# Performance work log

Hardware: AMD Instinct MI355X
Metric: run time of the kernel (lower is better)

Reference implementation:

```python
import jax, jax.numpy as jnp
import numpy as np

N = 10000
E = 160000
D_IN = 128
H = 1024
NUM_GRAPHS = 8
EPS = 1e-5


def setup_inputs() -> dict:
    key = jax.random.key(0)
    ks = jax.random.split(key, 24)
    x = jax.random.normal(ks[0], (N, D_IN), dtype=jnp.float32)
    edge_index = jax.random.randint(ks[1], (2, E), 0, N, dtype=jnp.int32)
    batch = jnp.sort(jax.random.randint(ks[2], (N,), 0, NUM_GRAPHS, dtype=jnp.int32))
    s = 0.02
    W1 = jax.random.normal(ks[3], (D_IN, H), dtype=jnp.float32) * s
    b1 = jnp.zeros((H,), jnp.float32)
    Wh = jax.random.normal(ks[4], (3, H, H), dtype=jnp.float32) * s
    bh = jnp.zeros((3, H), jnp.float32)
    ln_g = jnp.ones((4, H), jnp.float32)
    ln_b = jnp.zeros((4, H), jnp.float32)
    vW = jax.random.normal(ks[5], (6, H, H), dtype=jnp.float32) * s
    vb = jnp.zeros((6, H), jnp.float32)
    vWo = jax.random.normal(ks[6], (H, 1), dtype=jnp.float32) * s
    vbo = jnp.zeros((1,), jnp.float32)
    return {"x": x, "edge_index": edge_index, "batch": batch,
            "W1": W1, "b1": b1, "Wh": Wh, "bh": bh,
            "ln_g": ln_g, "ln_b": ln_b, "vW": vW, "vb": vb,
            "vWo": vWo, "vbo": vbo}


def _layer_norm(x, g, b):
    m = jnp.mean(x, axis=-1, keepdims=True)
    v = jnp.mean(jnp.square(x - m), axis=-1, keepdims=True)
    return (x - m) * jax.lax.rsqrt(v + EPS) * g + b


def reference(x, edge_index, batch, W1, b1, Wh, bh, ln_g, ln_b, vW, vb, vWo, vbo):
    # GCNConv: add self loops, symmetric normalization, x @ W, scatter-add at dst, + bias
    loops = jnp.arange(N, dtype=edge_index.dtype)
    src = jnp.concatenate([edge_index[0], loops])
    dst = jnp.concatenate([edge_index[1], loops])
    deg = jax.ops.segment_sum(jnp.ones_like(dst, dtype=x.dtype), dst, num_segments=N)
    dinv = jax.lax.rsqrt(jnp.maximum(deg, 1.0))
    norm = (dinv[src] * dinv[dst])[:, None]  # [E+N, 1]

    def gcn(h, W, b):
        h = h @ W                              # [N, H]
        msg = h[src] * norm                    # gather + scale [E+N, H]
        return jax.ops.segment_sum(msg, dst, num_segments=N) + b

    x1 = gcn(x, W1, b1)
    h = jax.nn.relu(_layer_norm(x1, ln_g[0], ln_b[0]))
    x2 = gcn(h, Wh[0], bh[0])
    h = jax.nn.relu(_layer_norm(x2 + x1, ln_g[1], ln_b[1]))
    x3 = gcn(h, Wh[1], bh[1])
    h = jax.nn.relu(_layer_norm(x3 + x1, ln_g[2], ln_b[2]))
    x4 = gcn(h, Wh[2], bh[2])
    node_embeddings = jax.nn.relu(_layer_norm(x4 + h, ln_g[3], ln_b[3]))

    # global mean pool per graph
    counts = jax.ops.segment_sum(jnp.ones((N,), x.dtype), batch, num_segments=NUM_GRAPHS)
    sums = jax.ops.segment_sum(node_embeddings, batch, num_segments=NUM_GRAPHS)
    graph_embedding = sums / jnp.maximum(counts, 1.0)[:, None]

    v = graph_embedding
    for i in range(6):
        v = jax.nn.relu(v @ vW[i] + vb[i])
    state_value = (v @ vWo + vbo).squeeze(-1)
    return node_embeddings, graph_embedding, state_value
```

## Files before the change

### kernel.cpp

```cpp
#include <hip/hip_runtime.h>
#include <stdint.h>

#define N_NODES 10000
#define E_EDGES 160000
#define DIN 128
#define H 1024
#define NUM_GRAPHS 8
#define LN_EPS 1e-5f

typedef unsigned short u16;
typedef __attribute__((ext_vector_type(8))) short short8;
typedef __attribute__((ext_vector_type(8))) unsigned short ushort8v;
typedef __attribute__((ext_vector_type(4))) float f32x4;

__device__ __forceinline__ float bf2f(u16 v) { return __uint_as_float(((unsigned)v) << 16); }
__device__ __forceinline__ u16 f2bf(float f) {
    unsigned u = __float_as_uint(f);
    u += 0x7fffu + ((u >> 16) & 1u);
    return (u16)(u >> 16);
}

__global__ void k_init(int* cnt, int* goff, float* __restrict__ gsum,
                       float* __restrict__ vbuf, const float* __restrict__ vb,
                       float* __restrict__ sbufs) {
    int i = blockIdx.x * 256 + threadIdx.x;
    if (i < N_NODES) cnt[i] = 0;
    if (i <= NUM_GRAPHS) goff[i] = 0;
    if (i < NUM_GRAPHS * H) gsum[i] = 0.f;
    if (i < 6 * H) {
        int il = i >> 10, j = i & (H - 1);
        float b = vb[il * H + j];
        float* base = vbuf + (size_t)(il + 1) * NUM_GRAPHS * H;
#pragma unroll
        for (int g = 0; g < NUM_GRAPHS; g++) base[g * H + j] = b;
    }
    for (int j = i; j < 3 * N_NODES * 2; j += 40 * 256) sbufs[j] = 0.f;
}

__global__ void k_setup(const int* __restrict__ dst, int* __restrict__ cnt,
                        const int* __restrict__ batch, int* __restrict__ goff,
                        const float* __restrict__ x, u16* __restrict__ xb) {
    int i = blockIdx.x * 256 + threadIdx.x;
    if (i < E_EDGES) atomicAdd(&cnt[dst[i]], 1);
    if (i < N_NODES) {
        int b0 = batch[i];
        int b1 = (i + 1 < N_NODES) ? batch[i + 1] : NUM_GRAPHS;
        for (int g = b0 + 1; g <= b1; g++) goff[g] = i + 1;
    }
    if (i < N_NODES * DIN) xb[i] = f2bf(x[i]);
}

__global__ __launch_bounds__(1024) void k_scan(const int* __restrict__ cnt, int* __restrict__ offs,
                                               int* __restrict__ cursor, float* __restrict__ dinv) {
    __shared__ int wsum[16];
    __shared__ int carry_s;
    int tid = threadIdx.x;
    int lane = tid & 63, wv = tid >> 6;
    if (tid == 0) carry_s = 0;
    __syncthreads();
    for (int base = 0; base < N_NODES; base += 1024) {
        int i = base + tid;
        int v = (i < N_NODES) ? cnt[i] : 0;
        int x = v;
#pragma unroll
        for (int off = 1; off < 64; off <<= 1) {
            int t = __shfl_up(x, off);
            if (lane >= off) x += t;
        }
        if (lane == 63) wsum[wv] = x;
        __syncthreads();
        int carry = carry_s;
        if (wv == 0) {
            int ws = (lane < 16) ? wsum[lane] : 0;
#pragma unroll
            for (int off = 1; off < 16; off <<= 1) {
                int t = __shfl_up(ws, off);
                if (lane >= off) ws += t;
            }
            if (lane < 16) wsum[lane] = ws;
        }
        __syncthreads();
        int wbase = (wv > 0) ? wsum[wv - 1] : 0;
        int incl = wbase + x;
        int excl = incl - v;
        if (i < N_NODES) {
            offs[i] = carry + excl;
            cursor[i] = carry + excl;
            dinv[i] = rsqrtf((float)(v + 1));
        }
        if (tid == 1023) carry_s = carry + incl;
        __syncthreads();
    }
    if (tid == 0) offs[N_NODES] = carry_s;
}

__global__ void k_fill(const int* __restrict__ src, const int* __restrict__ dst,
                       int* __restrict__ cursor, int* __restrict__ csr_src) {
    int e = blockIdx.x * 256 + threadIdx.x;
    if (e < E_EDGES) {
        int d = dst[e];
        int slot = atomicAdd(&cursor[d], 1);
        csr_src[slot] = src[e];
    }
}

__global__ void k_wprep(const float* __restrict__ W1, const float* __restrict__ Wh,
                        u16* __restrict__ Wt1, u16* __restrict__ Wt3) {
    __shared__ float tile[32][33];
    int z = blockIdx.z;
    const float* src;
    u16* dst;
    int R;
    if (z == 0) {
        if (blockIdx.y * 32 >= DIN) return;
        src = W1; dst = Wt1; R = DIN;
    } else {
        src = Wh + (size_t)(z - 1) * H * H;
        dst = Wt3 + (size_t)(z - 1) * H * H;
        R = H;
    }
    const int C = H;
    int tx = threadIdx.x, ty = threadIdx.y;
    int x = blockIdx.x * 32 + tx;
#pragma unroll
    for (int i = 0; i < 32; i += 8) {
        int y = blockIdx.y * 32 + ty + i;
        tile[ty + i][tx] = (y < R && x < C) ? src[(size_t)y * C + x] : 0.f;
    }
    __syncthreads();
    int xo = blockIdx.y * 32 + tx;
#pragma unroll
    for (int i = 0; i < 32; i += 8) {
        int yo = blockIdx.x * 32 + ty + i;
        if (yo < C && xo < R) dst[(size_t)yo * R + xo] = f2bf(tile[tx][ty + i]);
    }
}

__global__ __launch_bounds__(64) void k_agg_x(const u16* __restrict__ xb, const float* __restrict__ dinv,
                                              const int* __restrict__ offs, const int* __restrict__ csr_src,
                                              u16* __restrict__ xa) {
    __shared__ float s_dv[64];
    __shared__ int s_id[64];
    int d = blockIdx.x;
    int tid = threadIdx.x;
    int c = tid * 2;
    float dd = dinv[d];
    float a0, a1;
    {
        unsigned v = *(const unsigned*)(xb + (size_t)d * DIN + c);
        a0 = dd * bf2f((u16)(v & 0xffffu));
        a1 = dd * bf2f((u16)(v >> 16));
    }
    int beg = offs[d], end = offs[d + 1];
    for (int chunk = beg; chunk < end; chunk += 64) {
        int nthis = end - chunk;
        if (nthis > 64) nthis = 64;
        int np = (nthis + 7) & ~7;
        __syncthreads();
        if (tid < nthis) {
            int s = csr_src[chunk + tid];
            s_id[tid] = s;
            s_dv[tid] = dinv[s];
        } else if (tid < np) {
            s_id[tid] = d;
            s_dv[tid] = 0.f;
        }
        __syncthreads();
        for (int i = 0; i < np; i += 8) {
            unsigned v[8];
            float e[8];
#pragma unroll
            for (int u = 0; u < 8; u++) {
                int s = s_id[i + u];
                e[u] = s_dv[i + u];
                v[u] = *(const unsigned*)(xb + (size_t)s * DIN + c);
            }
#pragma unroll
            for (int u = 0; u < 8; u++) {
                a0 += e[u] * bf2f((u16)(v[u] & 0xffffu));
                a1 += e[u] * bf2f((u16)(v[u] >> 16));
            }
        }
    }
    a0 *= dd;
    a1 *= dd;
    unsigned o = ((unsigned)f2bf(a1) << 16) | (unsigned)f2bf(a0);
    *(unsigned*)(xa + (size_t)d * DIN + c) = o;
}

__global__ __launch_bounds__(128) void k_ln1(const u16* __restrict__ t, const float* __restrict__ bias,
                                             const float* __restrict__ gamma, const float* __restrict__ beta,
                                             u16* __restrict__ out_bf, u16* __restrict__ out_pre) {
    __shared__ float red1[2], red2[2];
    int d = blockIdx.x;
    int tid = threadIdx.x;
    int c = tid * 8;
    float x[8];
    {
        ushort8v v = *(const ushort8v*)(t + (size_t)d * H + c);
#pragma unroll
        for (int i = 0; i < 8; i++) x[i] = bf2f(v[i]) + bias[c + i];
    }
    {
        ushort8v p;
#pragma unroll
        for (int i = 0; i < 8; i++) p[i] = f2bf(x[i]);
        *(ushort8v*)(out_pre + (size_t)d * H + c) = p;
    }
    float s1 = 0.f, s2 = 0.f;
#pragma unroll
    for (int i = 0; i < 8; i++) { s1 += x[i]; s2 += x[i] * x[i]; }
#pragma unroll
    for (int off = 32; off > 0; off >>= 1) {
        s1 += __shfl_down(s1, off);
        s2 += __shfl_down(s2, off);
    }
    int lane = tid & 63, wv = tid >> 6;
    if (lane == 0) { red1[wv] = s1; red2[wv] = s2; }
    __syncthreads();
    float sum = red1[0] + red1[1];
    float ssq = red2[0] + red2[1];
    float mean = sum * (1.f / H);
    float var = fmaxf(ssq * (1.f / H) - mean * mean, 0.f);
    float inv = rsqrtf(var + LN_EPS);
    ushort8v o;
#pragma unroll
    for (int i = 0; i < 8; i++)
        o[i] = f2bf(fmaxf((x[i] - mean) * inv * gamma[c + i] + beta[c + i], 0.f));
    *(ushort8v*)(out_bf + (size_t)d * H + c) = o;
}

__global__ __launch_bounds__(256) void k_agg_col(const u16* __restrict__ t, const u16* __restrict__ resid,
                                                 const float* __restrict__ bias, const float* __restrict__ dinv,
                                                 const int* __restrict__ offs, const int* __restrict__ csr_src,
                                                 u16* __restrict__ abuf, float* __restrict__ sbuf) {
    int chunk = blockIdx.x & 7;
    int grp = threadIdx.x >> 4;
    int ln = threadIdx.x & 15;
    int d = (blockIdx.x >> 3) * 16 + grp;
    int col = chunk * 128 + ln * 8;
    const u16* tc = t + col;
    float dd = dinv[d];
    float a[8];
    {
        ushort8v v = *(const ushort8v*)(tc + (size_t)d * H);
#pragma unroll
        for (int i = 0; i < 8; i++) a[i] = dd * bf2f(v[i]);
    }
    int e = offs[d], end = offs[d + 1];
    for (; e + 8 <= end; e += 8) {
        int s[8];
        float w[8];
        ushort8v vv[8];
#pragma unroll
        for (int u = 0; u < 8; u++) s[u] = csr_src[e + u];
#pragma unroll
        for (int u = 0; u < 8; u++) {
            w[u] = dinv[s[u]];
            vv[u] = *(const ushort8v*)(tc + (size_t)s[u] * H);
        }
#pragma unroll
        for (int u = 0; u < 8; u++)
#pragma unroll
            for (int j = 0; j < 8; j++) a[j] += w[u] * bf2f(vv[u][j]);
    }
    for (; e + 2 <= end; e += 2) {
        int s0 = csr_src[e], s1 = csr_src[e + 1];
        float w0 = dinv[s0], w1 = dinv[s1];
        ushort8v v0 = *(const ushort8v*)(tc + (size_t)s0 * H);
        ushort8v v1 = *(const ushort8v*)(tc + (size_t)s1 * H);
#pragma unroll
        for (int j = 0; j < 8; j++) a[j] += w0 * bf2f(v0[j]) + w1 * bf2f(v1[j]);
    }
    if (e < end) {
        int s0 = csr_src[e];
        float w0 = dinv[s0];
        ushort8v v0 = *(const ushort8v*)(tc + (size_t)s0 * H);
#pragma unroll
        for (int j = 0; j < 8; j++) a[j] += w0 * bf2f(v0[j]);
    }
    float x[8];
    {
        ushort8v r = *(const ushort8v*)(resid + (size_t)d * H + col);
#pragma unroll
        for (int i = 0; i < 8; i++) x[i] = dd * a[i] + bias[col + i] + bf2f(r[i]);
    }
    ushort8v o;
#pragma unroll
    for (int i = 0; i < 8; i++) o[i] = f2bf(x[i]);
    *(ushort8v*)(abuf + (size_t)d * H + col) = o;
    float s1 = 0.f, s2 = 0.f;
#pragma unroll
    for (int i = 0; i < 8; i++) { s1 += x[i]; s2 += x[i] * x[i]; }
#pragma unroll
    for (int off = 1; off < 16; off <<= 1) {
        s1 += __shfl_xor(s1, off);
        s2 += __shfl_xor(s2, off);
    }
    if (ln == 0) {
        atomicAdd(&sbuf[d * 2], s1);
        atomicAdd(&sbuf[d * 2 + 1], s2);
    }
}

template <int MODE>
__global__ __launch_bounds__(256) void k_ln_apply(const u16* __restrict__ abuf, const float* __restrict__ sbuf,
                                                  const float* __restrict__ gamma, const float* __restrict__ beta,
                                                  u16* __restrict__ out_bf, float* __restrict__ out_f32) {
    int chunk = blockIdx.x & 7;
    int grp = threadIdx.x >> 4;
    int ln = threadIdx.x & 15;
    int d = (blockIdx.x >> 3) * 16 + grp;
    int col = chunk * 128 + ln * 8;
    float mean = sbuf[d * 2] * (1.f / H);
    float var = fmaxf(sbuf[d * 2 + 1] * (1.f / H) - mean * mean, 0.f);
    float inv = rsqrtf(var + LN_EPS);
    ushort8v v = *(const ushort8v*)(abuf + (size_t)d * H + col);
    float y[8];
#pragma unroll
    for (int i = 0; i < 8; i++)
        y[i] = fmaxf((bf2f(v[i]) - mean) * inv * gamma[col + i] + beta[col + i], 0.f);
    if (MODE == 2) {
        float4 o0 = {y[0], y[1], y[2], y[3]};
        float4 o1 = {y[4], y[5], y[6], y[7]};
        *(float4*)(out_f32 + (size_t)d * H + col) = o0;
        *(float4*)(out_f32 + (size_t)d * H + col + 4) = o1;
    } else {
        ushort8v o;
#pragma unroll
        for (int i = 0; i < 8; i++) o[i] = f2bf(y[i]);
        *(ushort8v*)(out_bf + (size_t)d * H + col) = o;
    }
}

typedef __attribute__((address_space(1))) const unsigned int gas_u32;
typedef __attribute__((address_space(3))) unsigned int las_u32;
__device__ __forceinline__ void gld_lds16(const void* g, void* l) {
    __builtin_amdgcn_global_load_lds((gas_u32*)g, (las_u32*)l, 16, 0, 0);
}

__global__ __launch_bounds__(256) void k_gemm(const u16* __restrict__ A, const u16* __restrict__ B,
                                              u16* __restrict__ C, int M, int Nn, int K) {
    __shared__ __align__(16) u16 sA[2][128 * 32];
    __shared__ __align__(16) u16 sB[2][128 * 32];
    int mtiles = (M + 127) >> 7;
    int L = blockIdx.x;
    int cls = L & 7;
    int s = L >> 3;
    int nt = s & 7;
    int mt = (s >> 3) * 8 + cls;
    if (mt >= mtiles) return;
    int m0 = mt << 7;
    int n0 = nt << 7;

    int tid = threadIdx.x;
    int lane = tid & 63;
    int w = tid >> 6;
    int wm = w >> 1, wn = w & 1;

    f32x4 zero = {0.f, 0.f, 0.f, 0.f};
    f32x4 acc[4][4];
#pragma unroll
    for (int i = 0; i < 4; i++)
#pragma unroll
        for (int j = 0; j < 4; j++) acc[i][j] = zero;

    int srow = w * 32 + (lane >> 2);
    int scol = (((lane & 3) ^ ((lane >> 3) & 3))) * 8;

    auto STAGE = [&](int p, int k0) {
#pragma unroll
        for (int q = 0; q < 2; q++) {
            int rA = m0 + srow + q * 16;
            rA = rA < M ? rA : M - 1;
            gld_lds16(A + (size_t)rA * K + k0 + scol, sA[p] + w * 1024 + q * 512);
            gld_lds16(B + (size_t)(n0 + srow + q * 16) * K + k0 + scol, sB[p] + w * 1024 + q * 512);
        }
    };

    int NK = K >> 5;
    STAGE(0, 0);
    __syncthreads();

    int rchunk = ((lane >> 4) ^ ((lane >> 1) & 3)) * 8;
    int arow = (wm * 64 + (lane & 15)) * 32 + rchunk;
    int brow = (wn * 64 + (lane & 15)) * 32 + rchunk;

    for (int kt = 0; kt < NK; kt++) {
        int cur = kt & 1;
        if (kt + 1 < NK) STAGE(cur ^ 1, (kt + 1) << 5);

        short8 af[4], bv[4];
#pragma unroll
        for (int mi = 0; mi < 4; mi++)
            af[mi] = *(const short8*)(sA[cur] + arow + mi * 16 * 32);
#pragma unroll
        for (int ni = 0; ni < 4; ni++)
            bv[ni] = *(const short8*)(sB[cur] + brow + ni * 16 * 32);
#pragma unroll
        for (int mi = 0; mi < 4; mi++)
#pragma unroll
            for (int ni = 0; ni < 4; ni++)
                acc[mi][ni] = __builtin_amdgcn_mfma_f32_16x16x32_bf16(af[mi], bv[ni], acc[mi][ni], 0, 0, 0);

        __syncthreads();
    }

    int rbase = m0 + wm * 64 + (lane >> 4) * 4;
    int cbase = n0 + wn * 64 + (lane & 15);
#pragma unroll
    for (int mi = 0; mi < 4; mi++) {
#pragma unroll
        for (int r = 0; r < 4; r++) {
            int row = rbase + mi * 16 + r;
            if (row < M) {
#pragma unroll
                for (int ni = 0; ni < 4; ni++)
                    C[(size_t)row * Nn + cbase + ni * 16] = f2bf(acc[mi][ni][r]);
            }
        }
    }
}

#define PC_NODES 16
__global__ __launch_bounds__(256) void k_pool_acc(const float* __restrict__ ne, const int* __restrict__ batch,
                                                  float* __restrict__ gsum) {
    int c = blockIdx.x * 256 + threadIdx.x;
    int nbeg = blockIdx.y * PC_NODES;
    int nend = nbeg + PC_NODES;
    if (nend > N_NODES) nend = N_NODES;
    float acc = 0.f;
    int curg = batch[nbeg];
    for (int n = nbeg; n < nend; n++) {
        int g = batch[n];
        if (g != curg) {
            atomicAdd(&gsum[curg * H + c], acc);
            acc = 0.f;
            curg = g;
        }
        acc += ne[(size_t)n * H + c];
    }
    atomicAdd(&gsum[curg * H + c], acc);
}

__global__ __launch_bounds__(256) void k_pool_fin(const float* __restrict__ gsum, const int* __restrict__ goff,
                                                  float* __restrict__ v0, float* __restrict__ ge_out) {
    int g = blockIdx.y;
    int c = blockIdx.x * 256 + threadIdx.x;
    float cntf = (float)(goff[g + 1] - goff[g]);
    float m = gsum[g * H + c] / fmaxf(cntf, 1.f);
    v0[g * H + c] = m;
    ge_out[(size_t)g * H + c] = m;
}

template <bool RELU_IN>
__global__ __launch_bounds__(256) void k_mlp_acc(const float* __restrict__ vin, const float* __restrict__ W,
                                                 float* __restrict__ vout) {
    __shared__ float sk[64];
    int g = blockIdx.y;
    int j = blockIdx.x * 256 + threadIdx.x;
    int k0 = blockIdx.z * 64;
    if (threadIdx.x < 64) {
        float v = vin[g * H + k0 + threadIdx.x];
        sk[threadIdx.x] = RELU_IN ? fmaxf(v, 0.f) : v;
    }
    __syncthreads();
    float acc = 0.f;
#pragma unroll
    for (int k = 0; k < 64; k++) acc += sk[k] * W[(size_t)(k0 + k) * H + j];
    atomicAdd(&vout[g * H + j], acc);
}

__global__ void k_head(const float* __restrict__ vin, const float* __restrict__ Wo,
                       const float* __restrict__ bo, float* __restrict__ out) {
    int g = blockIdx.x;
    int tid = threadIdx.x;
    float s = 0.f;
    for (int k = tid; k < H; k += 256) s += fmaxf(vin[g * H + k], 0.f) * Wo[k];
#pragma unroll
    for (int off = 32; off > 0; off >>= 1) s += __shfl_down(s, off);
    __shared__ float p[4];
    if ((tid & 63) == 0) p[tid >> 6] = s;
    __syncthreads();
    if (tid == 0) out[g] = p[0] + p[1] + p[2] + p[3] + bo[0];
}

extern "C" void kernel_launch(void* const* d_in, const int* in_sizes, int n_in,
                              void* d_out, int out_size, void* d_ws, size_t ws_size,
                              hipStream_t stream) {
    const float* x = (const float*)d_in[0];
    const int* ei = (const int*)d_in[1];
    const int* batch = (const int*)d_in[2];
    const float* W1 = (const float*)d_in[3];
    const float* b1 = (const float*)d_in[4];
    const float* Wh = (const float*)d_in[5];
    const float* bh = (const float*)d_in[6];
    const float* ln_g = (const float*)d_in[7];
    const float* ln_b = (const float*)d_in[8];
    const float* vW = (const float*)d_in[9];
    const float* vb = (const float*)d_in[10];
    const float* vWo = (const float*)d_in[11];
    const float* vbo = (const float*)d_in[12];
    const int* esrc = ei;
    const int* edst = ei + E_EDGES;

    char* ws = (char*)d_ws;
    size_t off = 0;
    auto carve = [&](size_t bytes) -> char* {
        char* p = ws + off;
        off += (bytes + 255) & ~(size_t)255;
        return p;
    };
    float* dinv = (float*)carve(N_NODES * 4);
    int* cnt = (int*)carve(N_NODES * 4);
    int* offs = (int*)carve((N_NODES + 1) * 4);
    int* cursor = (int*)carve(N_NODES * 4);
    int* csr_src = (int*)carve(E_EDGES * 4);
    int* goff = (int*)carve((NUM_GRAPHS + 1) * 4);
    float* gsum = (float*)carve(NUM_GRAPHS * H * 4);
    float* vbuf = (float*)carve((size_t)7 * NUM_GRAPHS * H * 4);
    float* sbufs = (float*)carve((size_t)3 * N_NODES * 2 * 4);
    u16* xb = (u16*)carve((size_t)N_NODES * DIN * 2);
    u16* xa = (u16*)carve((size_t)N_NODES * DIN * 2);
    u16* Wt1 = (u16*)carve((size_t)H * DIN * 2);
    u16* Wt3 = (u16*)carve((size_t)3 * H * H * 2);
    u16* tbuf = (u16*)carve((size_t)N_NODES * H * 2);
    u16* hbuf = (u16*)carve((size_t)N_NODES * H * 2);
    u16* x1buf = (u16*)carve((size_t)N_NODES * H * 2);
    u16* abuf = (u16*)carve((size_t)N_NODES * H * 2);

    float* out_ne = (float*)d_out;
    float* out_ge = out_ne + (size_t)N_NODES * H;
    float* out_sv = out_ge + (size_t)NUM_GRAPHS * H;

    k_init<<<(N_NODES + 255) / 256, 256, 0, stream>>>(cnt, goff, gsum, vbuf, vb, sbufs);
    k_setup<<<(N_NODES * DIN + 255) / 256, 256, 0, stream>>>(edst, cnt, batch, goff, x, xb);
    k_scan<<<1, 1024, 0, stream>>>(cnt, offs, cursor, dinv);
    k_fill<<<(E_EDGES + 255) / 256, 256, 0, stream>>>(esrc, edst, cursor, csr_src);
    k_wprep<<<dim3(H / 32, H / 32, 4), dim3(32, 8), 0, stream>>>(W1, Wh, Wt1, Wt3);

    int mtiles = (N_NODES + 127) / 128;
    int gemm_grid = 8 * 8 * ((mtiles + 7) / 8);
    int agg_grid = (N_NODES / 16) * 8;

    k_agg_x<<<N_NODES, 64, 0, stream>>>(xb, dinv, offs, csr_src, xa);
    k_gemm<<<gemm_grid, 256, 0, stream>>>(xa, Wt1, tbuf, N_NODES, H, DIN);
    k_ln1<<<N_NODES, 128, 0, stream>>>(tbuf, b1, ln_g, ln_b, hbuf, x1buf);

    k_gemm<<<gemm_grid, 256, 0, stream>>>(hbuf, Wt3, tbuf, N_NODES, H, H);
    k_agg_col<<<agg_grid, 256, 0, stream>>>(tbuf, x1buf, bh, dinv, offs, csr_src, abuf, sbufs);
    k_ln_apply<1><<<agg_grid, 256, 0, stream>>>(abuf, sbufs, ln_g + H, ln_b + H, hbuf, nullptr);

    k_gemm<<<gemm_grid, 256, 0, stream>>>(hbuf, Wt3 + (size_t)H * H, tbuf, N_NODES, H, H);
    k_agg_col<<<agg_grid, 256, 0, stream>>>(tbuf, x1buf, bh + H, dinv, offs, csr_src, abuf, sbufs + 2 * N_NODES);
    k_ln_apply<1><<<agg_grid, 256, 0, stream>>>(abuf, sbufs + 2 * N_NODES, ln_g + 2 * H, ln_b + 2 * H, hbuf, nullptr);

    k_gemm<<<gemm_grid, 256, 0, stream>>>(hbuf, Wt3 + (size_t)2 * H * H, tbuf, N_NODES, H, H);
    k_agg_col<<<agg_grid, 256, 0, stream>>>(tbuf, hbuf, bh + 2 * H, dinv, offs, csr_src, abuf, sbufs + 4 * N_NODES);
    k_ln_apply<2><<<agg_grid, 256, 0, stream>>>(abuf, sbufs + 4 * N_NODES, ln_g + 3 * H, ln_b + 3 * H, nullptr, out_ne);

    k_pool_acc<<<dim3(H / 256, (N_NODES + PC_NODES - 1) / PC_NODES), 256, 0, stream>>>(out_ne, batch, gsum);
    k_pool_fin<<<dim3(H / 256, NUM_GRAPHS), 256, 0, stream>>>(gsum, goff, vbuf, out_ge);

    dim3 mg(H / 256, NUM_GRAPHS, 16);
    k_mlp_acc<false><<<mg, 256, 0, stream>>>(vbuf, vW, vbuf + (size_t)1 * NUM_GRAPHS * H);
    for (int i = 1; i < 6; i++)
        k_mlp_acc<true><<<mg, 256, 0, stream>>>(vbuf + (size_t)i * NUM_GRAPHS * H, vW + (size_t)i * H * H,
                                                vbuf + (size_t)(i + 1) * NUM_GRAPHS * H);
    k_head<<<NUM_GRAPHS, 256, 0, stream>>>(vbuf + (size_t)6 * NUM_GRAPHS * H, vWo, vbo, out_sv);
}
```

Baseline: 466.9 us.

## Split edge lists across lane groups in aggregation and fuse mean-pool into LN

The aggregation kernel now assigns four destination nodes per wavefront and splits each node's edge list across four 16-lane groups, combining partial sums with cross-lane shuffles. This is meant to balance work across lanes and expose more memory parallelism per wave, at the cost of extra shuffles and idle lanes in the epilogue. Separately, the final LayerNorm-apply kernel now accumulates per-graph column sums in shared memory and atomically adds them to the global pool buffer. That removes the separate pooling kernel and its second read of the fp32 node embeddings, in exchange for shared-memory atomics.

```diff
diff --git a/kernel.cpp b/kernel.cpp
--- a/kernel.cpp
+++ b/kernel.cpp
@@ -235,82 +235,84 @@
                                                  const int* __restrict__ offs, const int* __restrict__ csr_src,
                                                  u16* __restrict__ abuf, float* __restrict__ sbuf) {
     int chunk = blockIdx.x & 7;
-    int grp = threadIdx.x >> 4;
-    int ln = threadIdx.x & 15;
-    int d = (blockIdx.x >> 3) * 16 + grp;
+    int lane = threadIdx.x & 63;
+    int wv = threadIdx.x >> 6;
+    int grp = lane >> 4;
+    int ln = lane & 15;
     int col = chunk * 128 + ln * 8;
     const u16* tc = t + col;
-    float dd = dinv[d];
-    float a[8];
-    {
-        ushort8v v = *(const ushort8v*)(tc + (size_t)d * H);
-#pragma unroll
-        for (int i = 0; i < 8; i++) a[i] = dd * bf2f(v[i]);
-    }
-    int e = offs[d], end = offs[d + 1];
-    for (; e + 8 <= end; e += 8) {
-        int s[8];
-        float w[8];
-        ushort8v vv[8];
-#pragma unroll
-        for (int u = 0; u < 8; u++) s[u] = csr_src[e + u];
-#pragma unroll
-        for (int u = 0; u < 8; u++) {
-            w[u] = dinv[s[u]];
-            vv[u] = *(const ushort8v*)(tc + (size_t)s[u] * H);
-        }
-#pragma unroll
-        for (int u = 0; u < 8; u++)
-#pragma unroll
-            for (int j = 0; j < 8; j++) a[j] += w[u] * bf2f(vv[u][j]);
-    }
-    for (; e + 2 <= end; e += 2) {
-        int s0 = csr_src[e], s1 = csr_src[e + 1];
-        float w0 = dinv[s0], w1 = dinv[s1];
-        ushort8v v0 = *(const ushort8v*)(tc + (size_t)s0 * H);
-        ushort8v v1 = *(const ushort8v*)(tc + (size_t)s1 * H);
-#pragma unroll
-        for (int j = 0; j < 8; j++) a[j] += w0 * bf2f(v0[j]) + w1 * bf2f(v1[j]);
-    }
-    if (e < end) {
-        int s0 = csr_src[e];
-        float w0 = dinv[s0];
-        ushort8v v0 = *(const ushort8v*)(tc + (size_t)s0 * H);
-#pragma unroll
-        for (int j = 0; j < 8; j++) a[j] += w0 * bf2f(v0[j]);
-    }
-    float x[8];
-    {
-        ushort8v r = *(const ushort8v*)(resid + (size_t)d * H + col);
-#pragma unroll
-        for (int i = 0; i < 8; i++) x[i] = dd * a[i] + bias[col + i] + bf2f(r[i]);
-    }
-    ushort8v o;
-#pragma unroll
-    for (int i = 0; i < 8; i++) o[i] = f2bf(x[i]);
-    *(ushort8v*)(abuf + (size_t)d * H + col) = o;
-    float s1 = 0.f, s2 = 0.f;
-#pragma unroll
-    for (int i = 0; i < 8; i++) { s1 += x[i]; s2 += x[i] * x[i]; }
-#pragma unroll
-    for (int off = 1; off < 16; off <<= 1) {
-        s1 += __shfl_xor(s1, off);
-        s2 += __shfl_xor(s2, off);
-    }
-    if (ln == 0) {
-        atomicAdd(&sbuf[d * 2], s1);
-        atomicAdd(&sbuf[d * 2 + 1], s2);
+    int dbase = (blockIdx.x >> 3) * 16 + wv * 4;
+#pragma unroll 1
+    for (int r = 0; r < 4; r++) {
+        int d = dbase + r;
+        int beg = offs[d];
+        int deg = offs[d + 1] - beg;
+        int e = beg + ((deg * grp) >> 2);
+        int e1 = beg + ((deg * (grp + 1)) >> 2);
+        float a[8];
+#pragma unroll
+        for (int i = 0; i < 8; i++) a[i] = 0.f;
+        for (; e + 4 <= e1; e += 4) {
+            int s0 = csr_src[e], s1 = csr_src[e + 1], s2 = csr_src[e + 2], s3 = csr_src[e + 3];
+            float w0 = dinv[s0], w1 = dinv[s1], w2 = dinv[s2], w3 = dinv[s3];
+            ushort8v v0 = *(const ushort8v*)(tc + (size_t)s0 * H);
+            ushort8v v1 = *(const ushort8v*)(tc + (size_t)s1 * H);
+            ushort8v v2 = *(const ushort8v*)(tc + (size_t)s2 * H);
+            ushort8v v3 = *(const ushort8v*)(tc + (size_t)s3 * H);
+#pragma unroll
+            for (int j = 0; j < 8; j++)
+                a[j] += w0 * bf2f(v0[j]) + w1 * bf2f(v1[j]) + w2 * bf2f(v2[j]) + w3 * bf2f(v3[j]);
+        }
+        for (; e < e1; e++) {
+            int s0 = csr_src[e];
+            float w0 = dinv[s0];
+            ushort8v v0 = *(const ushort8v*)(tc + (size_t)s0 * H);
+#pragma unroll
+            for (int j = 0; j < 8; j++) a[j] += w0 * bf2f(v0[j]);
+        }
+#pragma unroll
+        for (int j = 0; j < 8; j++) {
+            a[j] += __shfl_xor(a[j], 16);
+            a[j] += __shfl_xor(a[j], 32);
+        }
+        if (grp == 0) {
+            float dd = dinv[d];
+            ushort8v sv = *(const ushort8v*)(tc + (size_t)d * H);
+            ushort8v rv = *(const ushort8v*)(resid + (size_t)d * H + col);
+            float x[8];
+#pragma unroll
+            for (int i = 0; i < 8; i++)
+                x[i] = dd * (a[i] + dd * bf2f(sv[i])) + bias[col + i] + bf2f(rv[i]);
+            ushort8v o;
+#pragma unroll
+            for (int i = 0; i < 8; i++) o[i] = f2bf(x[i]);
+            *(ushort8v*)(abuf + (size_t)d * H + col) = o;
+            float s1 = 0.f, s2 = 0.f;
+#pragma unroll
+            for (int i = 0; i < 8; i++) { s1 += x[i]; s2 += x[i] * x[i]; }
+#pragma unroll
+            for (int off = 1; off < 16; off <<= 1) {
+                s1 += __shfl_xor(s1, off);
+                s2 += __shfl_xor(s2, off);
+            }
+            if (ln == 0) {
+                atomicAdd(&sbuf[d * 2], s1);
+                atomicAdd(&sbuf[d * 2 + 1], s2);
+            }
+        }
     }
 }
 
 template <int MODE>
 __global__ __launch_bounds__(256) void k_ln_apply(const u16* __restrict__ abuf, const float* __restrict__ sbuf,
                                                   const float* __restrict__ gamma, const float* __restrict__ beta,
-                                                  u16* __restrict__ out_bf, float* __restrict__ out_f32) {
+                                                  u16* __restrict__ out_bf, float* __restrict__ out_f32,
+                                                  const int* __restrict__ batch, float* __restrict__ gsum) {
     int chunk = blockIdx.x & 7;
     int grp = threadIdx.x >> 4;
     int ln = threadIdx.x & 15;
-    int d = (blockIdx.x >> 3) * 16 + grp;
+    int dtile = (blockIdx.x >> 3) * 16;
+    int d = dtile + grp;
     int col = chunk * 128 + ln * 8;
     float mean = sbuf[d * 2] * (1.f / H);
     float var = fmaxf(sbuf[d * 2 + 1] * (1.f / H) - mean * mean, 0.f);
@@ -325,6 +327,24 @@
         float4 o1 = {y[4], y[5], y[6], y[7]};
         *(float4*)(out_f32 + (size_t)d * H + col) = o0;
         *(float4*)(out_f32 + (size_t)d * H + col + 4) = o1;
+        __shared__ float sacc[2][128];
+        __shared__ int sg1;
+        int g0 = batch[dtile];
+        int g = batch[d];
+        if (threadIdx.x < 128) { sacc[0][threadIdx.x] = 0.f; sacc[1][threadIdx.x] = 0.f; }
+        if (threadIdx.x == 0) sg1 = -1;
+        __syncthreads();
+        int slot = (g != g0) ? 1 : 0;
+        if (slot && ln == 0) sg1 = g;
+        int lc = ln * 8;
+#pragma unroll
+        for (int i = 0; i < 8; i++) atomicAdd(&sacc[slot][lc + i], y[i]);
+        __syncthreads();
+        if (threadIdx.x < 128) {
+            atomicAdd(&gsum[g0 * H + chunk * 128 + threadIdx.x], sacc[0][threadIdx.x]);
+            int g1 = sg1;
+            if (g1 >= 0) atomicAdd(&gsum[g1 * H + chunk * 128 + threadIdx.x], sacc[1][threadIdx.x]);
+        }
     } else {
         ushort8v o;
 #pragma unroll
@@ -420,27 +440,6 @@
             }
         }
     }
-}
-
-#define PC_NODES 16
-__global__ __launch_bounds__(256) void k_pool_acc(const float* __restrict__ ne, const int* __restrict__ batch,
-                                                  float* __restrict__ gsum) {
-    int c = blockIdx.x * 256 + threadIdx.x;
-    int nbeg = blockIdx.y * PC_NODES;
-    int nend = nbeg + PC_NODES;
-    if (nend > N_NODES) nend = N_NODES;
-    float acc = 0.f;
-    int curg = batch[nbeg];
-    for (int n = nbeg; n < nend; n++) {
-        int g = batch[n];
-        if (g != curg) {
-            atomicAdd(&gsum[curg * H + c], acc);
-            acc = 0.f;
-            curg = g;
-        }
-        acc += ne[(size_t)n * H + c];
-    }
-    atomicAdd(&gsum[curg * H + c], acc);
 }
 
 __global__ __launch_bounds__(256) void k_pool_fin(const float* __restrict__ gsum, const int* __restrict__ goff,
@@ -549,17 +548,16 @@
 
     k_gemm<<<gemm_grid, 256, 0, stream>>>(hbuf, Wt3, tbuf, N_NODES, H, H);
     k_agg_col<<<agg_grid, 256, 0, stream>>>(tbuf, x1buf, bh, dinv, offs, csr_src, abuf, sbufs);
-    k_ln_apply<1><<<agg_grid, 256, 0, stream>>>(abuf, sbufs, ln_g + H, ln_b + H, hbuf, nullptr);
+    k_ln_apply<1><<<agg_grid, 256, 0, stream>>>(abuf, sbufs, ln_g + H, ln_b + H, hbuf, nullptr, nullptr, nullptr);
 
     k_gemm<<<gemm_grid, 256, 0, stream>>>(hbuf, Wt3 + (size_t)H * H, tbuf, N_NODES, H, H);
     k_agg_col<<<agg_grid, 256, 0, stream>>>(tbuf, x1buf, bh + H, dinv, offs, csr_src, abuf, sbufs + 2 * N_NODES);
-    k_ln_apply<1><<<agg_grid, 256, 0, stream>>>(abuf, sbufs + 2 * N_NODES, ln_g + 2 * H, ln_b + 2 * H, hbuf, nullptr);
+    k_ln_apply<1><<<agg_grid, 256, 0, stream>>>(abuf, sbufs + 2 * N_NODES, ln_g + 2 * H, ln_b + 2 * H, hbuf, nullptr, nullptr, nullptr);
 
     k_gemm<<<gemm_grid, 256, 0, stream>>>(hbuf, Wt3 + (size_t)2 * H * H, tbuf, N_NODES, H, H);
     k_agg_col<<<agg_grid, 256, 0, stream>>>(tbuf, hbuf, bh + 2 * H, dinv, offs, csr_src, abuf, sbufs + 4 * N_NODES);
-    k_ln_apply<2><<<agg_grid, 256, 0, stream>>>(abuf, sbufs + 4 * N_NODES, ln_g + 3 * H, ln_b + 3 * H, nullptr, out_ne);
-
-    k_pool_acc<<<dim3(H / 256, (N_NODES + PC_NODES - 1) / PC_NODES), 256, 0, stream>>>(out_ne, batch, gsum);
+    k_ln_apply<2><<<agg_grid, 256, 0, stream>>>(abuf, sbufs + 4 * N_NODES, ln_g + 3 * H, ln_b + 3 * H, nullptr, out_ne, batch, gsum);
+
     k_pool_fin<<<dim3(H / 256, NUM_GRAPHS), 256, 0, stream>>>(gsum, goff, vbuf, out_ge);
 
     dim3 mg(H / 256, NUM_GRAPHS, 16);
```

Result: slower. 539.1 us (+15.5%).
